# Optimization experiments

Measured on AMD Instinct MI355X. Metric: run time of the kernel, lower is better.

## Reference

```python
import jax, jax.numpy as jnp
import numpy as np

N_HARMONIC = 6
CONCAT = (3,)  # cfg.append_distance: concat embedding after this layer index
N_LAYERS = 8


def harmonic_embedding(x):
    # x: [N, 3] -> [N, 6*2*3 + 3] = [N, 39]
    freqs = 2.0 ** jnp.arange(N_HARMONIC, dtype=x.dtype)  # omega0 = 1.0, logspace
    embed = (x[..., None] * freqs).reshape(*x.shape[:-1], -1)  # [N, 18]
    return jnp.concatenate([jnp.sin(embed), jnp.cos(embed), x], axis=-1)


def setup_inputs() -> dict:
    key = jax.random.key(0)
    N, H, E = 262144, 256, 39
    ks = jax.random.split(key, 11)
    inp = {"points": jax.random.normal(ks[0], (N, 3), dtype=jnp.float32)}
    in_dims = [E, H, H, H, E + H, H, H, H]  # skip-concat before layer 4
    for i, d_in in enumerate(in_dims):
        scale = 1.0 / np.sqrt(d_in)
        inp[f"w{i}"] = jax.random.normal(ks[i + 1], (d_in, H), dtype=jnp.float32) * scale
        inp[f"b{i}"] = jnp.zeros((H,), dtype=jnp.float32)
    inp["wsdf"] = jax.random.normal(ks[9], (H, 1), dtype=jnp.float32) * (1.0 / np.sqrt(H))
    inp["bsdf"] = jnp.zeros((1,), dtype=jnp.float32)
    return inp


def reference(points, w0, b0, w1, b1, w2, b2, w3, b3, w4, b4, w5, b5, w6, b6, w7, b7, wsdf, bsdf):
    ws = [w0, w1, w2, w3, w4, w5, w6, w7]
    bs = [b0, b1, b2, b3, b4, b5, b6, b7]
    emb = harmonic_embedding(points.reshape(-1, 3))  # [N, 39]
    x = emb
    for i in range(N_LAYERS):
        x = jax.nn.relu(x @ ws[i] + bs[i])
        if i in CONCAT:
            x = jnp.concatenate([emb, x], axis=-1)  # torch.cat([add, xyz])
    return x @ wsdf + bsdf  # [N, 1] signed distance
```

## Files before the change

### kernel.cpp

```cpp
#include <hip/hip_runtime.h>
#include <hip/hip_fp16.h>

typedef _Float16 f16x8 __attribute__((ext_vector_type(8)));
typedef _Float16 f16x4 __attribute__((ext_vector_type(4)));
typedef _Float16 f16x2 __attribute__((ext_vector_type(2)));
typedef float    f32x16 __attribute__((ext_vector_type(16)));
typedef float    f32x4 __attribute__((ext_vector_type(4)));

struct LayerPtrs {
  const float* w[8];
  const float* b[8];
};

__global__ void prep_weights(LayerPtrs P, f16x8* __restrict__ wf) {
  int gid = blockIdx.x * 256 + threadIdx.x;
  if (gid >= 60416) return;
  const int OFF[9] = {0,1536,9728,17920,26112,35840,44032,52224,60416};
  int l = 0;
  while (gid >= OFF[l+1]) ++l;
  int f = gid - OFF[l];
  int lane = f & 63;
  int t = f >> 6;
  int mtile = t & 7;
  int kc = t >> 3;
  int col = mtile * 32 + (lane & 31);
  int kb  = (lane >> 5) * 8;
  const float* w = P.w[l];
  f16x8 v;
#pragma unroll
  for (int j = 0; j < 8; ++j) {
    float x = 0.f;
    if (l == 4) {
      if (kc < 3) {
        int k = kc * 16 + kb + j;
        if (k < 39) x = w[k * 256 + col];
      } else {
        int k = (kc - 3) * 16 + kb + j;
        x = w[(39 + k) * 256 + col];
      }
    } else if (l == 0) {
      int k = kc * 16 + kb + j;
      if (k < 39) x = w[k * 256 + col];
    } else {
      int k = kc * 16 + kb + j;
      x = w[k * 256 + col];
    }
    v[j] = (_Float16)x;
  }
  wf[gid] = v;
}

#define MFMA __builtin_amdgcn_mfma_f32_32x32x16_f16

template<int NKC, bool FIRST, int RSTRIDE>
__device__ __forceinline__ void mm(const f16x8* __restrict__ wb,
                                   const char* __restrict__ r0,
                                   int col0, int xr,
                                   f32x16 acc[2][2]) {
  f16x8 a0 = wb[0];
  f16x8 a1 = wb[64];
  f16x8 b0, b1;
  if (NKC > 1) { b0 = wb[512]; b1 = wb[576]; }
  int off0 = col0 ^ xr;
  f16x8 v0 = *(const f16x8*)(r0 + off0);
  f16x8 v1 = *(const f16x8*)(r0 + RSTRIDE + off0);
#pragma unroll
  for (int kc = 0; kc < NKC; ++kc) {
    f16x8 na0, na1, nv0, nv1;
    if (kc + 2 < NKC) {
      na0 = wb[(kc + 2) * 512];
      na1 = wb[(kc + 2) * 512 + 64];
    }
    if (kc + 1 < NKC) {
      int off = (col0 + 32 * (kc + 1)) ^ xr;
      nv0 = *(const f16x8*)(r0 + off);
      nv1 = *(const f16x8*)(r0 + RSTRIDE + off);
    }
    if (FIRST && kc == 0) {
      const f32x16 z = {};
      acc[0][0] = MFMA(a0, v0, z, 0, 0, 0);
      acc[0][1] = MFMA(a0, v1, z, 0, 0, 0);
      acc[1][0] = MFMA(a1, v0, z, 0, 0, 0);
      acc[1][1] = MFMA(a1, v1, z, 0, 0, 0);
    } else {
      acc[0][0] = MFMA(a0, v0, acc[0][0], 0, 0, 0);
      acc[0][1] = MFMA(a0, v1, acc[0][1], 0, 0, 0);
      acc[1][0] = MFMA(a1, v0, acc[1][0], 0, 0, 0);
      acc[1][1] = MFMA(a1, v1, acc[1][1], 0, 0, 0);
    }
    a0 = b0; a1 = b1; b0 = na0; b1 = na1;
    v0 = nv0; v1 = nv1;
  }
}

__device__ __forceinline__ f16x4 relu_cvt4(float a0, float a1, float a2, float a3) {
  f16x2 lo = __builtin_bit_cast(f16x2, __builtin_amdgcn_cvt_pkrtz(a0, a1));
  f16x2 hi = __builtin_bit_cast(f16x2, __builtin_amdgcn_cvt_pkrtz(a2, a3));
  union { f16x4 v; f16x2 h[2]; } u;
  u.h[0] = lo; u.h[1] = hi;
  f16x4 z = {};
  return __builtin_elementwise_max(u.v, z);
}

__device__ __forceinline__ void store_epi(f32x16 acc[2][2],
                                          const float* __restrict__ bias,
                                          int wg_h, int wg_p, int p0, int h,
                                          int xr, _Float16* __restrict__ Hs) {
  char* base = (char*)Hs + (wg_p * 64 + p0) * 512;
#pragma unroll
  for (int mt = 0; mt < 2; ++mt) {
#pragma unroll
    for (int g = 0; g < 4; ++g) {
      f32x4 q = *(const f32x4*)&bias[wg_h * 64 + mt * 32 + 8 * g + 4 * h];
      int bc = (128 * wg_h + 64 * mt + 8 * h + 16 * g) ^ xr;
#pragma unroll
      for (int nt = 0; nt < 2; ++nt) {
        f16x4 o = relu_cvt4(acc[mt][nt][4 * g + 0] + q[0],
                            acc[mt][nt][4 * g + 1] + q[1],
                            acc[mt][nt][4 * g + 2] + q[2],
                            acc[mt][nt][4 * g + 3] + q[3]);
        *(f16x4*)(base + nt * 32 * 512 + bc) = o;
      }
    }
  }
}

__global__ __launch_bounds__(512, 4)
void mlp_fused(const float* __restrict__ points,
               LayerPtrs P,
               const f16x8* __restrict__ wf,
               const float* __restrict__ wsdf,
               const float* __restrict__ bsdf,
               float* __restrict__ out) {
  __shared__ __align__(16) _Float16 Hs[128 * 256];
  __shared__ __align__(16) _Float16 Es[128 * 64];
  const int tid = threadIdx.x;
  const int blk = blockIdx.x;

  const int lane = tid & 63;
  const int w    = tid >> 6;
  const int wg_h = w & 3;
  const int wg_p = w >> 2;
  const int p0   = lane & 31;
  const int h    = lane >> 5;
  const int xr   = (p0 & 7) << 4;
  const int col0 = 16 * h;

  const f16x8* wb = wf + wg_h * 128 + lane;

  {
    int p = tid & 127, part = tid >> 7;
    char* Erow = (char*)Es + p * 128;
    int xp = (p & 7) << 4;
    if (part < 3) {
      float x = points[(blk * 128 + p) * 3 + part];
      _Float16 sv[6], cv[6];
      float fr = 1.f;
#pragma unroll
      for (int k = 0; k < 6; ++k) {
        float e = x * fr;
        sv[k] = (_Float16)__sinf(e);
        cv[k] = (_Float16)__cosf(e);
        fr *= 2.f;
      }
#pragma unroll
      for (int k = 0; k < 6; k += 2) {
        f16x2 s2 = {sv[k], sv[k + 1]};
        f16x2 c2 = {cv[k], cv[k + 1]};
        *(f16x2*)(Erow + ((2 * (6 * part + k)) ^ xp)) = s2;
        *(f16x2*)(Erow + ((2 * (18 + 6 * part + k)) ^ xp)) = c2;
      }
      *(_Float16*)(Erow + ((2 * (36 + part)) ^ xp)) = (_Float16)x;
    } else {
      f16x4 z4 = {};
      *(_Float16*)(Erow + (78 ^ xp)) = (_Float16)0.f;
      *(f16x4*)(Erow + (80 ^ xp)) = z4;
      *(f16x4*)(Erow + (88 ^ xp)) = z4;
    }
  }
  __syncthreads();

  const char* hR = (const char*)Hs + (wg_p * 64 + p0) * 512;
  const char* eR = (const char*)Es + (wg_p * 64 + p0) * 128;

  f32x16 acc[2][2];

  mm<3, true, 4096>(wb, eR, col0, xr, acc);
  store_epi(acc, P.b[0], wg_h, wg_p, p0, h, xr, Hs);
  __syncthreads();

  const int WOFF[8] = {0, 1536, 9728, 17920, 26112, 35840, 44032, 52224};

#pragma unroll
  for (int l = 1; l < 4; ++l) {
    mm<16, true, 16384>(wb + WOFF[l], hR, col0, xr, acc);
    __syncthreads();
    store_epi(acc, P.b[l], wg_h, wg_p, p0, h, xr, Hs);
    __syncthreads();
  }

  {
    mm<3, true, 4096>(wb + 26112, eR, col0, xr, acc);
    mm<16, false, 16384>(wb + 27648, hR, col0, xr, acc);
    __syncthreads();
    store_epi(acc, P.b[4], wg_h, wg_p, p0, h, xr, Hs);
    __syncthreads();
  }

#pragma unroll
  for (int l = 5; l < 7; ++l) {
    mm<16, true, 16384>(wb + WOFF[l], hR, col0, xr, acc);
    __syncthreads();
    store_epi(acc, P.b[l], wg_h, wg_p, p0, h, xr, Hs);
    __syncthreads();
  }

  mm<16, true, 16384>(wb + 52224, hR, col0, xr, acc);
  {
    float part0 = 0.f, part1 = 0.f;
    const float* b7 = P.b[7];
#pragma unroll
    for (int mt = 0; mt < 2; ++mt) {
#pragma unroll
      for (int g = 0; g < 4; ++g) {
        int idx = wg_h * 64 + mt * 32 + 8 * g + 4 * h;
        f32x4 qb = *(const f32x4*)&b7[idx];
        f32x4 qw = *(const f32x4*)&wsdf[idx];
#pragma unroll
        for (int r = 0; r < 4; ++r) {
          part0 += fmaxf(acc[mt][0][4 * g + r] + qb[r], 0.f) * qw[r];
          part1 += fmaxf(acc[mt][1][4 * g + r] + qb[r], 0.f) * qw[r];
        }
      }
    }
    float* PB = (float*)Es;
    PB[(wg_h * 2 + h) * 128 + wg_p * 64 + p0]      = part0;
    PB[(wg_h * 2 + h) * 128 + wg_p * 64 + 32 + p0] = part1;
    __syncthreads();
    if (tid < 128) {
      float s = bsdf[0];
#pragma unroll
      for (int j = 0; j < 8; ++j) s += PB[j * 128 + tid];
      out[blk * 128 + tid] = s;
    }
  }
}

extern "C" void kernel_launch(void* const* d_in, const int* in_sizes, int n_in,
                              void* d_out, int out_size, void* d_ws, size_t ws_size,
                              hipStream_t stream) {
  const float* points = (const float*)d_in[0];
  LayerPtrs P;
  for (int i = 0; i < 8; ++i) {
    P.w[i] = (const float*)d_in[1 + 2 * i];
    P.b[i] = (const float*)d_in[2 + 2 * i];
  }
  const float* wsdf = (const float*)d_in[17];
  const float* bsdf = (const float*)d_in[18];
  f16x8* wf = (f16x8*)d_ws;

  int N = in_sizes[0] / 3;
  prep_weights<<<236, 256, 0, stream>>>(P, wf);
  mlp_fused<<<N / 128, 512, 0, stream>>>(points, P, wf, wsdf, bsdf, (float*)d_out);
}
```

Before: 327.6 us.

## Double per-wave output tile width, halve block to 256 threads

Each wave now computes 128 output columns (4 M-tiles) instead of 64, so every LDS activation fragment feeds twice as many MFMAs and the weight loads per point are amortized better. Blocks shrink from 8 to 4 waves still covering 128 points, and the embedding work is redistributed across the 2 thread halves. This doubles accumulator register pressure (128 acc VGPRs) and lowers waves per block, which may reduce latency hiding.

```diff
diff --git a/kernel.cpp b/kernel.cpp
--- a/kernel.cpp
+++ b/kernel.cpp
@@ -56,20 +56,21 @@
 __device__ __forceinline__ void mm(const f16x8* __restrict__ wb,
                                    const char* __restrict__ r0,
                                    int col0, int xr,
-                                   f32x16 acc[2][2]) {
-  f16x8 a0 = wb[0];
-  f16x8 a1 = wb[64];
-  f16x8 b0, b1;
-  if (NKC > 1) { b0 = wb[512]; b1 = wb[576]; }
+                                   f32x16 acc[4][2]) {
+  f16x8 a0 = wb[0], a1 = wb[64], a2 = wb[128], a3 = wb[192];
+  f16x8 b0, b1, b2, b3;
+  if (NKC > 1) { b0 = wb[512]; b1 = wb[576]; b2 = wb[640]; b3 = wb[704]; }
   int off0 = col0 ^ xr;
   f16x8 v0 = *(const f16x8*)(r0 + off0);
   f16x8 v1 = *(const f16x8*)(r0 + RSTRIDE + off0);
 #pragma unroll
   for (int kc = 0; kc < NKC; ++kc) {
-    f16x8 na0, na1, nv0, nv1;
+    f16x8 na0, na1, na2, na3, nv0, nv1;
     if (kc + 2 < NKC) {
       na0 = wb[(kc + 2) * 512];
       na1 = wb[(kc + 2) * 512 + 64];
+      na2 = wb[(kc + 2) * 512 + 128];
+      na3 = wb[(kc + 2) * 512 + 192];
     }
     if (kc + 1 < NKC) {
       int off = (col0 + 32 * (kc + 1)) ^ xr;
@@ -82,13 +83,22 @@
       acc[0][1] = MFMA(a0, v1, z, 0, 0, 0);
       acc[1][0] = MFMA(a1, v0, z, 0, 0, 0);
       acc[1][1] = MFMA(a1, v1, z, 0, 0, 0);
+      acc[2][0] = MFMA(a2, v0, z, 0, 0, 0);
+      acc[2][1] = MFMA(a2, v1, z, 0, 0, 0);
+      acc[3][0] = MFMA(a3, v0, z, 0, 0, 0);
+      acc[3][1] = MFMA(a3, v1, z, 0, 0, 0);
     } else {
       acc[0][0] = MFMA(a0, v0, acc[0][0], 0, 0, 0);
       acc[0][1] = MFMA(a0, v1, acc[0][1], 0, 0, 0);
       acc[1][0] = MFMA(a1, v0, acc[1][0], 0, 0, 0);
       acc[1][1] = MFMA(a1, v1, acc[1][1], 0, 0, 0);
-    }
-    a0 = b0; a1 = b1; b0 = na0; b1 = na1;
+      acc[2][0] = MFMA(a2, v0, acc[2][0], 0, 0, 0);
+      acc[2][1] = MFMA(a2, v1, acc[2][1], 0, 0, 0);
+      acc[3][0] = MFMA(a3, v0, acc[3][0], 0, 0, 0);
+      acc[3][1] = MFMA(a3, v1, acc[3][1], 0, 0, 0);
+    }
+    a0 = b0; a1 = b1; a2 = b2; a3 = b3;
+    b0 = na0; b1 = na1; b2 = na2; b3 = na3;
     v0 = nv0; v1 = nv1;
   }
 }
@@ -102,17 +112,17 @@
   return __builtin_elementwise_max(u.v, z);
 }
 
-__device__ __forceinline__ void store_epi(f32x16 acc[2][2],
+__device__ __forceinline__ void store_epi(f32x16 acc[4][2],
                                           const float* __restrict__ bias,
                                           int wg_h, int wg_p, int p0, int h,
                                           int xr, _Float16* __restrict__ Hs) {
   char* base = (char*)Hs + (wg_p * 64 + p0) * 512;
 #pragma unroll
-  for (int mt = 0; mt < 2; ++mt) {
+  for (int mt = 0; mt < 4; ++mt) {
 #pragma unroll
     for (int g = 0; g < 4; ++g) {
-      f32x4 q = *(const f32x4*)&bias[wg_h * 64 + mt * 32 + 8 * g + 4 * h];
-      int bc = (128 * wg_h + 64 * mt + 8 * h + 16 * g) ^ xr;
+      f32x4 q = *(const f32x4*)&bias[wg_h * 128 + mt * 32 + 8 * g + 4 * h];
+      int bc = (256 * wg_h + 64 * mt + 16 * g + 8 * h) ^ xr;
 #pragma unroll
       for (int nt = 0; nt < 2; ++nt) {
         f16x4 o = relu_cvt4(acc[mt][nt][4 * g + 0] + q[0],
@@ -125,7 +135,28 @@
   }
 }
 
-__global__ __launch_bounds__(512, 4)
+__device__ __forceinline__ void emb_channel(char* __restrict__ Erow, int xp,
+                                            int c, float x) {
+  _Float16 sv[6], cv[6];
+  float fr = 1.f;
+#pragma unroll
+  for (int k = 0; k < 6; ++k) {
+    float e = x * fr;
+    sv[k] = (_Float16)__sinf(e);
+    cv[k] = (_Float16)__cosf(e);
+    fr *= 2.f;
+  }
+#pragma unroll
+  for (int k = 0; k < 6; k += 2) {
+    f16x2 s2 = {sv[k], sv[k + 1]};
+    f16x2 c2 = {cv[k], cv[k + 1]};
+    *(f16x2*)(Erow + ((2 * (6 * c + k)) ^ xp)) = s2;
+    *(f16x2*)(Erow + ((2 * (18 + 6 * c + k)) ^ xp)) = c2;
+  }
+  *(_Float16*)(Erow + ((2 * (36 + c)) ^ xp)) = (_Float16)x;
+}
+
+__global__ __launch_bounds__(256, 2)
 void mlp_fused(const float* __restrict__ points,
                LayerPtrs P,
                const f16x8* __restrict__ wf,
@@ -139,39 +170,25 @@
 
   const int lane = tid & 63;
   const int w    = tid >> 6;
-  const int wg_h = w & 3;
-  const int wg_p = w >> 2;
+  const int wg_h = w >> 1;
+  const int wg_p = w & 1;
   const int p0   = lane & 31;
   const int h    = lane >> 5;
   const int xr   = (p0 & 7) << 4;
   const int col0 = 16 * h;
 
-  const f16x8* wb = wf + wg_h * 128 + lane;
+  const f16x8* wb = wf + wg_h * 256 + lane;
 
   {
     int p = tid & 127, part = tid >> 7;
     char* Erow = (char*)Es + p * 128;
     int xp = (p & 7) << 4;
-    if (part < 3) {
-      float x = points[(blk * 128 + p) * 3 + part];
-      _Float16 sv[6], cv[6];
-      float fr = 1.f;
-#pragma unroll
-      for (int k = 0; k < 6; ++k) {
-        float e = x * fr;
-        sv[k] = (_Float16)__sinf(e);
-        cv[k] = (_Float16)__cosf(e);
-        fr *= 2.f;
-      }
-#pragma unroll
-      for (int k = 0; k < 6; k += 2) {
-        f16x2 s2 = {sv[k], sv[k + 1]};
-        f16x2 c2 = {cv[k], cv[k + 1]};
-        *(f16x2*)(Erow + ((2 * (6 * part + k)) ^ xp)) = s2;
-        *(f16x2*)(Erow + ((2 * (18 + 6 * part + k)) ^ xp)) = c2;
-      }
-      *(_Float16*)(Erow + ((2 * (36 + part)) ^ xp)) = (_Float16)x;
+    const float* pp = &points[(blk * 128 + p) * 3];
+    if (part == 0) {
+      emb_channel(Erow, xp, 0, pp[0]);
+      emb_channel(Erow, xp, 1, pp[1]);
     } else {
+      emb_channel(Erow, xp, 2, pp[2]);
       f16x4 z4 = {};
       *(_Float16*)(Erow + (78 ^ xp)) = (_Float16)0.f;
       *(f16x4*)(Erow + (80 ^ xp)) = z4;
@@ -183,7 +200,7 @@
   const char* hR = (const char*)Hs + (wg_p * 64 + p0) * 512;
   const char* eR = (const char*)Es + (wg_p * 64 + p0) * 128;
 
-  f32x16 acc[2][2];
+  f32x16 acc[4][2];
 
   mm<3, true, 4096>(wb, eR, col0, xr, acc);
   store_epi(acc, P.b[0], wg_h, wg_p, p0, h, xr, Hs);
@@ -220,10 +237,10 @@
     float part0 = 0.f, part1 = 0.f;
     const float* b7 = P.b[7];
 #pragma unroll
-    for (int mt = 0; mt < 2; ++mt) {
+    for (int mt = 0; mt < 4; ++mt) {
 #pragma unroll
       for (int g = 0; g < 4; ++g) {
-        int idx = wg_h * 64 + mt * 32 + 8 * g + 4 * h;
+        int idx = wg_h * 128 + mt * 32 + 8 * g + 4 * h;
         f32x4 qb = *(const f32x4*)&b7[idx];
         f32x4 qw = *(const f32x4*)&wsdf[idx];
 #pragma unroll
@@ -240,7 +257,7 @@
     if (tid < 128) {
       float s = bsdf[0];
 #pragma unroll
-      for (int j = 0; j < 8; ++j) s += PB[j * 128 + tid];
+      for (int j = 0; j < 4; ++j) s += PB[j * 128 + tid];
       out[blk * 128 + tid] = s;
     }
   }
@@ -261,5 +278,5 @@
 
   int N = in_sizes[0] / 3;
   prep_weights<<<236, 256, 0, stream>>>(P, wf);
-  mlp_fused<<<N / 128, 512, 0, stream>>>(points, P, wf, wsdf, bsdf, (float*)d_out);
-}
+  mlp_fused<<<N / 128, 256, 0, stream>>>(points, P, wf, wsdf, bsdf, (float*)d_out);
+}
```

Measured after the change: 473.5 us. 44.5% more time.
